# Performance work log

Measured on AMD Instinct MI355X. Metric: run time of the kernel, lower is better.

## Reference

```python
import jax, jax.numpy as jnp
import numpy as np

B, S, D = 2, 2048, 1024
H, DK = 16, 64  # n_heads, d_k == d_v


def setup_inputs() -> dict:
    key = jax.random.key(0)
    ks = jax.random.split(key, 12)
    sd = 1.0 / np.sqrt(D)
    inp = {
        "Q": jax.random.normal(ks[0], (B, S, D), jnp.float32),
        "K": jax.random.normal(ks[1], (B, S, D), jnp.float32),
        "V": jax.random.normal(ks[2], (B, S, D), jnp.float32),
        "attn_mask": jax.random.randint(ks[3], (B, S, S), 0, 2).astype(bool),
        "Wq": jax.random.normal(ks[4], (D, H * DK), jnp.float32) * sd,
        "bq": jnp.zeros((H * DK,), jnp.float32),
        "Wk": jax.random.normal(ks[5], (D, H * DK), jnp.float32) * sd,
        "bk": jnp.zeros((H * DK,), jnp.float32),
        "Wv": jax.random.normal(ks[6], (D, H * DK), jnp.float32) * sd,
        "bv": jnp.zeros((H * DK,), jnp.float32),
        "Wo": jax.random.normal(ks[7], (H * DK, D), jnp.float32) * sd,
        "bo": jnp.zeros((D,), jnp.float32),
        "ln_g": jnp.ones((D,), jnp.float32),
        "ln_b": jnp.zeros((D,), jnp.float32),
    }
    return inp


def _layer_norm(x, g, b, eps=1e-5):
    mu = jnp.mean(x, axis=-1, keepdims=True)
    var = jnp.var(x, axis=-1, keepdims=True)
    return (x - mu) * jax.lax.rsqrt(var + eps) * g + b


def reference(Q, K, V, attn_mask, Wq, bq, Wk, bk, Wv, bv, Wo, bo, ln_g, ln_b):
    # NOTE: faithful to the source — K and V projections are computed from Q.
    residual = Q
    q = (Q @ Wq + bq).reshape(B, S, H, DK).transpose(0, 2, 1, 3)  # [B,H,S,DK]
    k = (Q @ Wk + bk).reshape(B, S, H, DK).transpose(0, 2, 1, 3)
    v = (Q @ Wv + bv).reshape(B, S, H, DK).transpose(0, 2, 1, 3)
    scale = 1.0 / np.sqrt(DK)
    scores = jnp.einsum("bhqd,bhkd->bhqk", q, k) * scale  # [B,H,S,S]
    scores = jnp.where(attn_mask[:, None, :, :], jnp.float32(-1e9), scores)
    attn = jax.nn.softmax(scores, axis=-1)
    context = jnp.einsum("bhqk,bhkd->bhqd", attn, v)
    context = context.transpose(0, 2, 1, 3).reshape(B, S, H * DK)
    output = context @ Wo + bo
    return _layer_norm(output + residual, ln_g, ln_b), attn
```

## Files before the change

kernel.cpp:

```cpp
#include <hip/hip_runtime.h>
#include <stdint.h>

typedef unsigned short u16;
typedef short bf16x8 __attribute__((ext_vector_type(8)));
typedef float f32x4 __attribute__((ext_vector_type(4)));

static __device__ __forceinline__ u16 f2b(float f) {
    uint32_t u = __float_as_uint(f);
    uint32_t r = (u + 0x7fffu + ((u >> 16) & 1u)) >> 16;
    return (u16)r;
}
static __device__ __forceinline__ float b2f(u16 u) {
    union { float f; uint32_t i; } x; x.i = ((uint32_t)u) << 16; return x.f;
}

#define GLOAD16(g, l)                                                        \
    __builtin_amdgcn_global_load_lds(                                        \
        (const __attribute__((address_space(1))) uint32_t*)(g),              \
        (__attribute__((address_space(3))) uint32_t*)(l), 16, 0, 0)

__global__ __launch_bounds__(256) void pack_mask_k(const int* __restrict__ mask,
                                                   unsigned long long* __restrict__ bits) {
    const int row = blockIdx.x;
    const int wave = threadIdx.x >> 6, lane = threadIdx.x & 63;
    const int* mrow = mask + (size_t)row * 2048;
#pragma unroll
    for (int it = 0; it < 8; ++it) {
        int col = it * 256 + threadIdx.x;
        unsigned long long b = __ballot(mrow[col] != 0);
        if (lane == 0) bits[(size_t)row * 32 + it * 4 + wave] = b;
    }
}

__global__ __launch_bounds__(256) void transpose_w_k(const float* __restrict__ Wq, const float* __restrict__ Wk,
                                                     const float* __restrict__ Wv, const float* __restrict__ Wo,
                                                     u16* __restrict__ WtAll) {
    __shared__ u16 t[32][36];
    const float* W = blockIdx.z == 0 ? Wq : blockIdx.z == 1 ? Wk : blockIdx.z == 2 ? Wv : Wo;
    u16* out = WtAll + (size_t)blockIdx.z * (1024u * 1024u);
    const int r = threadIdx.x >> 3, c4 = (threadIdx.x & 7) * 4;
    float4 v = *(const float4*)(W + (size_t)(blockIdx.y * 32 + r) * 1024 + blockIdx.x * 32 + c4);
    t[r][c4 + 0] = f2b(v.x); t[r][c4 + 1] = f2b(v.y); t[r][c4 + 2] = f2b(v.z); t[r][c4 + 3] = f2b(v.w);
    __syncthreads();
    ushort4 o;
    o.x = t[c4 + 0][r]; o.y = t[c4 + 1][r]; o.z = t[c4 + 2][r]; o.w = t[c4 + 3][r];
    *(ushort4*)(out + (size_t)(blockIdx.x * 32 + r) * 1024 + blockIdx.y * 32 + c4) = o;
}

__global__ __launch_bounds__(256) void qcvt_k(const float* __restrict__ Q, u16* __restrict__ qbf) {
    const size_t i = ((size_t)blockIdx.x * 256 + threadIdx.x) * 8;
    float4 a = *(const float4*)(Q + i);
    float4 b = *(const float4*)(Q + i + 4);
    bf16x8 o;
    o[0] = (short)f2b(a.x); o[1] = (short)f2b(a.y); o[2] = (short)f2b(a.z); o[3] = (short)f2b(a.w);
    o[4] = (short)f2b(b.x); o[5] = (short)f2b(b.y); o[6] = (short)f2b(b.z); o[7] = (short)f2b(b.w);
    *(bf16x8*)(qbf + i) = o;
}

__global__ __launch_bounds__(256) void gemm_qkv_k(const u16* __restrict__ Abf, const u16* __restrict__ WtAll,
                                                  const float* __restrict__ bq, const float* __restrict__ bk,
                                                  const float* __restrict__ bv,
                                                  u16* __restrict__ q_ws, u16* __restrict__ k_ws,
                                                  u16* __restrict__ v_ws) {
    __shared__ u16 Asm[128 * 32];
    __shared__ u16 Bsm[128 * 32];
    const int tid = threadIdx.x;
    const int wave = tid >> 6, lane = tid & 63, quad = lane >> 4, l16 = lane & 15;
    const int wr = wave >> 1, wc = wave & 1;
    const int m0 = blockIdx.y * 128, n0 = blockIdx.x * 128;

    const u16* Ag = Abf + (size_t)(m0 + (tid >> 2)) * 1024 + (tid & 3) * 8;
    const u16* Bg = WtAll + (size_t)(n0 + (tid >> 2)) * 1024 + (tid & 3) * 8;

    const f32x4 zero = {0.f, 0.f, 0.f, 0.f};
    f32x4 acc[4][4];
#pragma unroll
    for (int i = 0; i < 4; ++i)
#pragma unroll
        for (int j = 0; j < 4; ++j) acc[i][j] = zero;

    for (int k0 = 0; k0 < 1024; k0 += 32) {
        GLOAD16(Ag + k0, &Asm[tid * 8]);
        GLOAD16(Ag + k0 + (size_t)64 * 1024, &Asm[2048 + tid * 8]);
        GLOAD16(Bg + k0, &Bsm[tid * 8]);
        GLOAD16(Bg + k0 + (size_t)64 * 1024, &Bsm[2048 + tid * 8]);
        __syncthreads();
        bf16x8 a[4], b[4];
#pragma unroll
        for (int i = 0; i < 4; ++i) {
            a[i] = *(const bf16x8*)&Asm[(wr * 64 + i * 16 + l16) * 32 + quad * 8];
            b[i] = *(const bf16x8*)&Bsm[(wc * 64 + i * 16 + l16) * 32 + quad * 8];
        }
#pragma unroll
        for (int mi = 0; mi < 4; ++mi)
#pragma unroll
            for (int ni = 0; ni < 4; ++ni)
                acc[mi][ni] = __builtin_amdgcn_mfma_f32_16x16x32_bf16(a[mi], b[ni], acc[mi][ni], 0, 0, 0);
        __syncthreads();
    }

    const int z = n0 >> 10;
    const float* bias = z == 0 ? bq : z == 1 ? bk : bv;
    u16* out = z == 0 ? q_ws : z == 1 ? k_ws : v_ws;
    const float oscale = (z == 0) ? 0.18033688011112042f : 1.0f;
#pragma unroll
    for (int ni = 0; ni < 4; ++ni) {
        const int n = n0 + wc * 64 + ni * 16 + l16;
        const int nn = n & 1023, h = nn >> 6, d = nn & 63;
        const float bsf = bias[nn];
#pragma unroll
        for (int mi = 0; mi < 4; ++mi)
#pragma unroll
            for (int r = 0; r < 4; ++r) {
                const int m = m0 + wr * 64 + mi * 16 + quad * 4 + r;
                const int bb = m >> 11, s = m & 2047;
                out[((size_t)(bb * 16 + h) * 2048 + s) * 64 + d] = f2b((acc[mi][ni][r] + bsf) * oscale);
            }
    }
}

__global__ __launch_bounds__(256) void vtr_k(const u16* __restrict__ v_ws, u16* __restrict__ vT) {
    __shared__ u16 t[32][36];
    const int bh = blockIdx.z, s0 = blockIdx.x * 32, d0 = blockIdx.y * 32;
    const int r = threadIdx.x >> 3, c4 = (threadIdx.x & 7) * 4;
    ushort4 v = *(const ushort4*)(v_ws + ((size_t)bh * 2048 + s0 + r) * 64 + d0 + c4);
    t[r][c4 + 0] = v.x; t[r][c4 + 1] = v.y; t[r][c4 + 2] = v.z; t[r][c4 + 3] = v.w;
    __syncthreads();
    ushort4 o;
    o.x = t[c4 + 0][r]; o.y = t[c4 + 1][r]; o.z = t[c4 + 2][r]; o.w = t[c4 + 3][r];
    *(ushort4*)(vT + ((size_t)bh * 64 + d0 + r) * 2048 + s0 + c4) = o;
}

__global__ __launch_bounds__(256) void attn_k(const u16* __restrict__ q_ws, const u16* __restrict__ k_ws,
                                              const u16* __restrict__ vT,
                                              const unsigned long long* __restrict__ mbits,
                                              float* __restrict__ attn_out, u16* __restrict__ ctx_ws) {
    const int bh = blockIdx.y, b = bh >> 4, h = bh & 15;
    const int q0 = blockIdx.x * 64;
    const int tid = threadIdx.x;
    const int wave = tid >> 6, lane = tid & 63, quad = lane >> 4, l16 = lane & 15;

    __shared__ u16 Ksm[64][72];
    __shared__ u16 Vsm[64][72];
    __shared__ u16 Psm[4][16][72];

    const u16* qp = q_ws + ((size_t)bh * 2048 + q0 + wave * 16 + l16) * 64;
    const bf16x8 aq0 = *(const bf16x8*)(qp + quad * 8);
    const bf16x8 aq1 = *(const bf16x8*)(qp + 32 + quad * 8);

    const size_t mbase = ((size_t)b * 2048 + q0 + wave * 16 + quad * 4) * 32;

    const int r0 = tid >> 3, c0 = (tid & 7) * 8;
    const u16* kgb = k_ws + (size_t)bh * 2048 * 64;
    const u16* vtg = vT + (size_t)bh * 64 * 2048;

    const f32x4 zero = {0.f, 0.f, 0.f, 0.f};
    float lsum[4] = {0.f, 0.f, 0.f, 0.f};

    for (int kt = 0; kt < 32; ++kt) {
        const int s0 = kt * 64;
        *(bf16x8*)&Ksm[r0][c0] = *(const bf16x8*)(kgb + (size_t)(s0 + r0) * 64 + c0);
        *(bf16x8*)&Ksm[r0 + 32][c0] = *(const bf16x8*)(kgb + (size_t)(s0 + r0 + 32) * 64 + c0);
        __syncthreads();
        f32x4 sc[4];
#pragma unroll
        for (int nt = 0; nt < 4; ++nt) {
            sc[nt] = zero;
            bf16x8 bk0 = *(const bf16x8*)&Ksm[nt * 16 + l16][quad * 8];
            bf16x8 bk1 = *(const bf16x8*)&Ksm[nt * 16 + l16][32 + quad * 8];
            sc[nt] = __builtin_amdgcn_mfma_f32_16x16x32_bf16(aq0, bk0, sc[nt], 0, 0, 0);
            sc[nt] = __builtin_amdgcn_mfma_f32_16x16x32_bf16(aq1, bk1, sc[nt], 0, 0, 0);
        }
        unsigned long long mw[4];
#pragma unroll
        for (int r = 0; r < 4; ++r) mw[r] = mbits[mbase + (size_t)r * 32 + kt];
#pragma unroll
        for (int nt = 0; nt < 4; ++nt)
#pragma unroll
            for (int r = 0; r < 4; ++r) {
                const int bit = (int)((mw[r] >> (nt * 16 + l16)) & 1ull);
                lsum[r] += bit ? 0.f : exp2f(sc[nt][r]);
            }
        __syncthreads();
    }
#pragma unroll
    for (int r = 0; r < 4; ++r) {
#pragma unroll
        for (int off = 1; off < 16; off <<= 1) lsum[r] += __shfl_xor(lsum[r], off, 64);
    }
    float rl[4];
#pragma unroll
    for (int r = 0; r < 4; ++r) rl[r] = 1.0f / lsum[r];

    f32x4 cacc[4];
#pragma unroll
    for (int i = 0; i < 4; ++i) cacc[i] = zero;

    for (int kt = 0; kt < 32; ++kt) {
        const int s0 = kt * 64;
        *(bf16x8*)&Ksm[r0][c0] = *(const bf16x8*)(kgb + (size_t)(s0 + r0) * 64 + c0);
        *(bf16x8*)&Ksm[r0 + 32][c0] = *(const bf16x8*)(kgb + (size_t)(s0 + r0 + 32) * 64 + c0);
        *(bf16x8*)&Vsm[r0][c0] = *(const bf16x8*)(vtg + (size_t)r0 * 2048 + s0 + c0);
        *(bf16x8*)&Vsm[r0 + 32][c0] = *(const bf16x8*)(vtg + (size_t)(r0 + 32) * 2048 + s0 + c0);
        __syncthreads();

        f32x4 sc[4];
#pragma unroll
        for (int nt = 0; nt < 4; ++nt) {
            sc[nt] = zero;
            bf16x8 bk0 = *(const bf16x8*)&Ksm[nt * 16 + l16][quad * 8];
            bf16x8 bk1 = *(const bf16x8*)&Ksm[nt * 16 + l16][32 + quad * 8];
            sc[nt] = __builtin_amdgcn_mfma_f32_16x16x32_bf16(aq0, bk0, sc[nt], 0, 0, 0);
            sc[nt] = __builtin_amdgcn_mfma_f32_16x16x32_bf16(aq1, bk1, sc[nt], 0, 0, 0);
        }
        unsigned long long mw[4];
#pragma unroll
        for (int r = 0; r < 4; ++r) mw[r] = mbits[mbase + (size_t)r * 32 + kt];
#pragma unroll
        for (int nt = 0; nt < 4; ++nt)
#pragma unroll
            for (int r = 0; r < 4; ++r) {
                const int bit = (int)((mw[r] >> (nt * 16 + l16)) & 1ull);
                const float p = bit ? 0.f : exp2f(sc[nt][r]) * rl[r];
                Psm[wave][quad * 4 + r][nt * 16 + l16] = f2b(p);
            }
#pragma unroll
        for (int j = 0; j < 4; ++j) {
            const int pr = j * 4 + (lane >> 4), pc = (lane & 15) * 4;
            ushort4 pv = *(const ushort4*)&Psm[wave][pr][pc];
            float4 pf;
            pf.x = b2f(pv.x); pf.y = b2f(pv.y); pf.z = b2f(pv.z); pf.w = b2f(pv.w);
            float* ap = attn_out + ((size_t)bh * 2048 + q0 + wave * 16 + pr) * 2048 + s0 + pc;
            *(float4*)ap = pf;
        }
        bf16x8 pa0 = *(const bf16x8*)&Psm[wave][l16][quad * 8];
        bf16x8 pa1 = *(const bf16x8*)&Psm[wave][l16][32 + quad * 8];
#pragma unroll
        for (int dt = 0; dt < 4; ++dt) {
            bf16x8 bv0 = *(const bf16x8*)&Vsm[dt * 16 + l16][quad * 8];
            bf16x8 bv1 = *(const bf16x8*)&Vsm[dt * 16 + l16][32 + quad * 8];
            cacc[dt] = __builtin_amdgcn_mfma_f32_16x16x32_bf16(pa0, bv0, cacc[dt], 0, 0, 0);
            cacc[dt] = __builtin_amdgcn_mfma_f32_16x16x32_bf16(pa1, bv1, cacc[dt], 0, 0, 0);
        }
        __syncthreads();
    }

#pragma unroll
    for (int dt = 0; dt < 4; ++dt) {
        const int d = dt * 16 + l16;
#pragma unroll
        for (int r = 0; r < 4; ++r) {
            const int s = q0 + wave * 16 + quad * 4 + r;
            ctx_ws[((size_t)b * 2048 + s) * 1024 + h * 64 + d] = f2b(cacc[dt][r]);
        }
    }
}

__global__ __launch_bounds__(256) void out_proj_k(const u16* __restrict__ Ctx, const u16* __restrict__ WtO,
                                                  const float* __restrict__ bo, const float* __restrict__ Qin,
                                                  float* __restrict__ ln_in) {
    __shared__ u16 Asm[128 * 32];
    __shared__ u16 Bsm[128 * 32];
    const int tid = threadIdx.x;
    const int wave = tid >> 6, lane = tid & 63, quad = lane >> 4, l16 = lane & 15;
    const int wr = wave >> 1, wc = wave & 1;
    const int m0 = blockIdx.y * 128, n0 = blockIdx.x * 128;

    const u16* Ag = Ctx + (size_t)(m0 + (tid >> 2)) * 1024 + (tid & 3) * 8;
    const u16* Bg = WtO + (size_t)(n0 + (tid >> 2)) * 1024 + (tid & 3) * 8;

    const f32x4 zero = {0.f, 0.f, 0.f, 0.f};
    f32x4 acc[4][4];
#pragma unroll
    for (int i = 0; i < 4; ++i)
#pragma unroll
        for (int j = 0; j < 4; ++j) acc[i][j] = zero;

    for (int k0 = 0; k0 < 1024; k0 += 32) {
        GLOAD16(Ag + k0, &Asm[tid * 8]);
        GLOAD16(Ag + k0 + (size_t)64 * 1024, &Asm[2048 + tid * 8]);
        GLOAD16(Bg + k0, &Bsm[tid * 8]);
        GLOAD16(Bg + k0 + (size_t)64 * 1024, &Bsm[2048 + tid * 8]);
        __syncthreads();
        bf16x8 a[4], b[4];
#pragma unroll
        for (int i = 0; i < 4; ++i) {
            a[i] = *(const bf16x8*)&Asm[(wr * 64 + i * 16 + l16) * 32 + quad * 8];
            b[i] = *(const bf16x8*)&Bsm[(wc * 64 + i * 16 + l16) * 32 + quad * 8];
        }
#pragma unroll
        for (int mi = 0; mi < 4; ++mi)
#pragma unroll
            for (int ni = 0; ni < 4; ++ni)
                acc[mi][ni] = __builtin_amdgcn_mfma_f32_16x16x32_bf16(a[mi], b[ni], acc[mi][ni], 0, 0, 0);
        __syncthreads();
    }
#pragma unroll
    for (int ni = 0; ni < 4; ++ni) {
        const int n = n0 + wc * 64 + ni * 16 + l16;
        const float bsf = bo[n];
#pragma unroll
        for (int mi = 0; mi < 4; ++mi)
#pragma unroll
            for (int r = 0; r < 4; ++r) {
                const int m = m0 + wr * 64 + mi * 16 + quad * 4 + r;
                ln_in[(size_t)m * 1024 + n] = acc[mi][ni][r] + bsf + Qin[(size_t)m * 1024 + n];
            }
    }
}

__global__ __launch_bounds__(256) void layernorm_k(const float* __restrict__ x, const float* __restrict__ g,
                                                   const float* __restrict__ bta, float* __restrict__ out) {
    const int row = blockIdx.x, tid = threadIdx.x;
    const float4 v = *(const float4*)(x + (size_t)row * 1024 + tid * 4);
    float s = v.x + v.y + v.z + v.w;
    float sq = v.x * v.x + v.y * v.y + v.z * v.z + v.w * v.w;
#pragma unroll
    for (int off = 32; off; off >>= 1) {
        s += __shfl_xor(s, off, 64);
        sq += __shfl_xor(sq, off, 64);
    }
    __shared__ float ss[4], ssq[4];
    const int wave = tid >> 6, lane = tid & 63;
    if (lane == 0) { ss[wave] = s; ssq[wave] = sq; }
    __syncthreads();
    const float S = ss[0] + ss[1] + ss[2] + ss[3];
    const float SQ = ssq[0] + ssq[1] + ssq[2] + ssq[3];
    const float mu = S * (1.f / 1024.f);
    const float rs = rsqrtf(SQ * (1.f / 1024.f) - mu * mu + 1e-5f);
    const float* vf = (const float*)&v;
    float4 o;
    float tmp[4];
#pragma unroll
    for (int j = 0; j < 4; ++j) {
        const int c = tid * 4 + j;
        tmp[j] = (vf[j] - mu) * rs * g[c] + bta[c];
    }
    o.x = tmp[0]; o.y = tmp[1]; o.z = tmp[2]; o.w = tmp[3];
    *(float4*)(out + (size_t)row * 1024 + tid * 4) = o;
}

extern "C" void kernel_launch(void* const* d_in, const int* in_sizes, int n_in,
                              void* d_out, int out_size, void* d_ws, size_t ws_size,
                              hipStream_t stream) {
    const float* Q  = (const float*)d_in[0];
    const int* mask = (const int*)d_in[3];
    const float* Wq = (const float*)d_in[4];
    const float* bq = (const float*)d_in[5];
    const float* Wk = (const float*)d_in[6];
    const float* bk = (const float*)d_in[7];
    const float* Wv = (const float*)d_in[8];
    const float* bv = (const float*)d_in[9];
    const float* Wo = (const float*)d_in[10];
    const float* bo = (const float*)d_in[11];
    const float* g  = (const float*)d_in[12];
    const float* be = (const float*)d_in[13];

    char* ws = (char*)d_ws;
    u16* WtAll = (u16*)(ws);
    u16* q_ws  = (u16*)(ws + ((size_t)8  << 20));
    u16* k_ws  = (u16*)(ws + ((size_t)16 << 20));
    u16* v_ws  = (u16*)(ws + ((size_t)24 << 20));
    u16* c_ws  = (u16*)(ws + ((size_t)32 << 20));
    u16* qbf   = (u16*)(ws + ((size_t)40 << 20));
    u16* vT    = (u16*)(ws + ((size_t)40 << 20));
    float* ln_in = (float*)(ws + ((size_t)40 << 20));
    unsigned long long* mbits = (unsigned long long*)(ws + ((size_t)56 << 20));

    float* out_ln = (float*)d_out;
    float* out_at = (float*)d_out + (size_t)2 * 2048 * 1024;

    transpose_w_k<<<dim3(32, 32, 4), dim3(256), 0, stream>>>(Wq, Wk, Wv, Wo, WtAll);
    pack_mask_k<<<dim3(4096), dim3(256), 0, stream>>>(mask, mbits);
    qcvt_k<<<dim3(2048), dim3(256), 0, stream>>>(Q, qbf);
    gemm_qkv_k<<<dim3(24, 32), dim3(256), 0, stream>>>(qbf, WtAll, bq, bk, bv, q_ws, k_ws, v_ws);
    vtr_k<<<dim3(64, 2, 32), dim3(256), 0, stream>>>(v_ws, vT);
    attn_k<<<dim3(32, 32), dim3(256), 0, stream>>>(q_ws, k_ws, vT, mbits, out_at, c_ws);
    out_proj_k<<<dim3(8, 32), dim3(256), 0, stream>>>(c_ws, WtAll + (size_t)3 * 1024 * 1024, bo, Q, ln_in);
    layernorm_k<<<dim3(4096), dim3(256), 0, stream>>>(ln_in, g, be, out_ln);
    (void)in_sizes; (void)n_in; (void)out_size; (void)ws_size;
}
```

Measured before the change: 837.5 us.

## Load K/V MFMA operands directly from global, drop LDS staging and barriers

The attention kernel no longer stages K and transposed V tiles through shared memory with __syncthreads. Each wave now loads its MFMA B-operands straight from global memory, counting on L1/L2 to serve the data that all four waves share. The grid mapping is swapped so that consecutive blocks cover the same batch-head, which should improve L2 reuse of K and V. s_setprio is raised around the MFMA sections. The risk is extra global/L1 traffic and exposed load latency with no explicit prefetch, in exchange for removing barrier stalls and LDS traffic.

```diff
diff --git a/kernel.cpp b/kernel.cpp
--- a/kernel.cpp
+++ b/kernel.cpp
@@ -135,13 +135,11 @@
                                               const u16* __restrict__ vT,
                                               const unsigned long long* __restrict__ mbits,
                                               float* __restrict__ attn_out, u16* __restrict__ ctx_ws) {
-    const int bh = blockIdx.y, b = bh >> 4, h = bh & 15;
-    const int q0 = blockIdx.x * 64;
+    const int bh = blockIdx.x, b = bh >> 4;
+    const int q0 = blockIdx.y * 64;
     const int tid = threadIdx.x;
     const int wave = tid >> 6, lane = tid & 63, quad = lane >> 4, l16 = lane & 15;
 
-    __shared__ u16 Ksm[64][72];
-    __shared__ u16 Vsm[64][72];
     __shared__ u16 Psm[4][16][72];
 
     const u16* qp = q_ws + ((size_t)bh * 2048 + q0 + wave * 16 + l16) * 64;
@@ -150,7 +148,6 @@
 
     const size_t mbase = ((size_t)b * 2048 + q0 + wave * 16 + quad * 4) * 32;
 
-    const int r0 = tid >> 3, c0 = (tid & 7) * 8;
     const u16* kgb = k_ws + (size_t)bh * 2048 * 64;
     const u16* vtg = vT + (size_t)bh * 64 * 2048;
 
@@ -158,19 +155,18 @@
     float lsum[4] = {0.f, 0.f, 0.f, 0.f};
 
     for (int kt = 0; kt < 32; ++kt) {
-        const int s0 = kt * 64;
-        *(bf16x8*)&Ksm[r0][c0] = *(const bf16x8*)(kgb + (size_t)(s0 + r0) * 64 + c0);
-        *(bf16x8*)&Ksm[r0 + 32][c0] = *(const bf16x8*)(kgb + (size_t)(s0 + r0 + 32) * 64 + c0);
-        __syncthreads();
+        const u16* kp = kgb + (size_t)kt * 64 * 64 + (size_t)l16 * 64 + quad * 8;
         f32x4 sc[4];
+        __builtin_amdgcn_s_setprio(1);
 #pragma unroll
         for (int nt = 0; nt < 4; ++nt) {
+            bf16x8 bk0 = *(const bf16x8*)(kp + nt * 1024);
+            bf16x8 bk1 = *(const bf16x8*)(kp + nt * 1024 + 32);
             sc[nt] = zero;
-            bf16x8 bk0 = *(const bf16x8*)&Ksm[nt * 16 + l16][quad * 8];
-            bf16x8 bk1 = *(const bf16x8*)&Ksm[nt * 16 + l16][32 + quad * 8];
             sc[nt] = __builtin_amdgcn_mfma_f32_16x16x32_bf16(aq0, bk0, sc[nt], 0, 0, 0);
             sc[nt] = __builtin_amdgcn_mfma_f32_16x16x32_bf16(aq1, bk1, sc[nt], 0, 0, 0);
         }
+        __builtin_amdgcn_s_setprio(0);
         unsigned long long mw[4];
 #pragma unroll
         for (int r = 0; r < 4; ++r) mw[r] = mbits[mbase + (size_t)r * 32 + kt];
@@ -181,7 +177,6 @@
                 const int bit = (int)((mw[r] >> (nt * 16 + l16)) & 1ull);
                 lsum[r] += bit ? 0.f : exp2f(sc[nt][r]);
             }
-        __syncthreads();
     }
 #pragma unroll
     for (int r = 0; r < 4; ++r) {
@@ -198,21 +193,18 @@
 
     for (int kt = 0; kt < 32; ++kt) {
         const int s0 = kt * 64;
-        *(bf16x8*)&Ksm[r0][c0] = *(const bf16x8*)(kgb + (size_t)(s0 + r0) * 64 + c0);
-        *(bf16x8*)&Ksm[r0 + 32][c0] = *(const bf16x8*)(kgb + (size_t)(s0 + r0 + 32) * 64 + c0);
-        *(bf16x8*)&Vsm[r0][c0] = *(const bf16x8*)(vtg + (size_t)r0 * 2048 + s0 + c0);
-        *(bf16x8*)&Vsm[r0 + 32][c0] = *(const bf16x8*)(vtg + (size_t)(r0 + 32) * 2048 + s0 + c0);
-        __syncthreads();
-
+        const u16* kp = kgb + (size_t)s0 * 64 + (size_t)l16 * 64 + quad * 8;
         f32x4 sc[4];
+        __builtin_amdgcn_s_setprio(1);
 #pragma unroll
         for (int nt = 0; nt < 4; ++nt) {
+            bf16x8 bk0 = *(const bf16x8*)(kp + nt * 1024);
+            bf16x8 bk1 = *(const bf16x8*)(kp + nt * 1024 + 32);
             sc[nt] = zero;
-            bf16x8 bk0 = *(const bf16x8*)&Ksm[nt * 16 + l16][quad * 8];
-            bf16x8 bk1 = *(const bf16x8*)&Ksm[nt * 16 + l16][32 + quad * 8];
             sc[nt] = __builtin_amdgcn_mfma_f32_16x16x32_bf16(aq0, bk0, sc[nt], 0, 0, 0);
             sc[nt] = __builtin_amdgcn_mfma_f32_16x16x32_bf16(aq1, bk1, sc[nt], 0, 0, 0);
         }
+        __builtin_amdgcn_s_setprio(0);
         unsigned long long mw[4];
 #pragma unroll
         for (int r = 0; r < 4; ++r) mw[r] = mbits[mbase + (size_t)r * 32 + kt];
@@ -235,16 +227,19 @@
         }
         bf16x8 pa0 = *(const bf16x8*)&Psm[wave][l16][quad * 8];
         bf16x8 pa1 = *(const bf16x8*)&Psm[wave][l16][32 + quad * 8];
+        const u16* vp = vtg + (size_t)l16 * 2048 + s0 + quad * 8;
+        __builtin_amdgcn_s_setprio(1);
 #pragma unroll
         for (int dt = 0; dt < 4; ++dt) {
-            bf16x8 bv0 = *(const bf16x8*)&Vsm[dt * 16 + l16][quad * 8];
-            bf16x8 bv1 = *(const bf16x8*)&Vsm[dt * 16 + l16][32 + quad * 8];
+            bf16x8 bv0 = *(const bf16x8*)(vp + (size_t)dt * 16 * 2048);
+            bf16x8 bv1 = *(const bf16x8*)(vp + (size_t)dt * 16 * 2048 + 32);
             cacc[dt] = __builtin_amdgcn_mfma_f32_16x16x32_bf16(pa0, bv0, cacc[dt], 0, 0, 0);
             cacc[dt] = __builtin_amdgcn_mfma_f32_16x16x32_bf16(pa1, bv1, cacc[dt], 0, 0, 0);
         }
-        __syncthreads();
-    }
-
+        __builtin_amdgcn_s_setprio(0);
+    }
+
+    const int h = bh & 15;
 #pragma unroll
     for (int dt = 0; dt < 4; ++dt) {
         const int d = dt * 16 + l16;
```

Result: slower. 1.109 ms (+32.4%).

## Double-buffer K/V tiles via async global-to-LDS loads with XOR swizzle

Applied to the files above, without the earlier changes.

Replaces the register-staged K and V tile loads in the attention kernel with global_load_lds copies into double-buffered, XOR-swizzled LDS tiles. The next tile is prefetched while the current one is consumed, which is meant to hide global load latency. The unpadded layout relies on the swizzle to avoid LDS bank conflicts. The grid axes are also swapped so consecutive blocks walk heads first, which changes L2 locality for the mask bits and K/V. There is one barrier per iteration, and the async copy relies on that barrier for ordering. This may race if the loads are not waited on (vmcnt) before the barrier.

```diff
diff --git a/kernel.cpp b/kernel.cpp
--- a/kernel.cpp
+++ b/kernel.cpp
@@ -131,18 +131,42 @@
     *(ushort4*)(vT + ((size_t)bh * 64 + d0 + r) * 2048 + s0 + c4) = o;
 }
 
+static __device__ __forceinline__ bf16x8 ld_swz(const u16* tile, int row, int cb) {
+    const int off = row * 128 + (cb ^ ((row & 7) << 4));
+    return *(const bf16x8*)((const char*)tile + off);
+}
+
 __global__ __launch_bounds__(256) void attn_k(const u16* __restrict__ q_ws, const u16* __restrict__ k_ws,
                                               const u16* __restrict__ vT,
                                               const unsigned long long* __restrict__ mbits,
                                               float* __restrict__ attn_out, u16* __restrict__ ctx_ws) {
-    const int bh = blockIdx.y, b = bh >> 4, h = bh & 15;
-    const int q0 = blockIdx.x * 64;
+    const int bh = blockIdx.x, b = bh >> 4, h = bh & 15;
+    const int q0 = blockIdx.y * 64;
     const int tid = threadIdx.x;
     const int wave = tid >> 6, lane = tid & 63, quad = lane >> 4, l16 = lane & 15;
 
-    __shared__ u16 Ksm[64][72];
-    __shared__ u16 Vsm[64][72];
+    __shared__ u16 Ksm[2][64 * 64];
+    __shared__ u16 Vsm[2][64 * 64];
     __shared__ u16 Psm[4][16][72];
+
+    const int st_row = tid >> 3;
+    const int st_sw = ((tid & 7) * 16) ^ ((st_row & 7) << 4);
+
+    const char* kgb = (const char*)(k_ws + (size_t)bh * 2048 * 64);
+    const char* vgb = (const char*)(vT + (size_t)bh * 64 * 2048);
+
+#define STAGE_K(buf, kt)                                                                   \
+    {                                                                                      \
+        const char* _s = kgb + (size_t)(kt) * 8192 + (size_t)st_row * 128 + st_sw;         \
+        GLOAD16(_s, &Ksm[buf][tid * 8]);                                                   \
+        GLOAD16(_s + 32 * 128, &Ksm[buf][2048 + tid * 8]);                                 \
+    }
+#define STAGE_V(buf, kt)                                                                   \
+    {                                                                                      \
+        const char* _s = vgb + (size_t)(kt) * 128 + (size_t)st_row * 4096 + st_sw;         \
+        GLOAD16(_s, &Vsm[buf][tid * 8]);                                                   \
+        GLOAD16(_s + (size_t)32 * 4096, &Vsm[buf][2048 + tid * 8]);                        \
+    }
 
     const u16* qp = q_ws + ((size_t)bh * 2048 + q0 + wave * 16 + l16) * 64;
     const bf16x8 aq0 = *(const bf16x8*)(qp + quad * 8);
@@ -150,24 +174,20 @@
 
     const size_t mbase = ((size_t)b * 2048 + q0 + wave * 16 + quad * 4) * 32;
 
-    const int r0 = tid >> 3, c0 = (tid & 7) * 8;
-    const u16* kgb = k_ws + (size_t)bh * 2048 * 64;
-    const u16* vtg = vT + (size_t)bh * 64 * 2048;
-
     const f32x4 zero = {0.f, 0.f, 0.f, 0.f};
     float lsum[4] = {0.f, 0.f, 0.f, 0.f};
 
+    STAGE_K(0, 0);
+    __syncthreads();
     for (int kt = 0; kt < 32; ++kt) {
-        const int s0 = kt * 64;
-        *(bf16x8*)&Ksm[r0][c0] = *(const bf16x8*)(kgb + (size_t)(s0 + r0) * 64 + c0);
-        *(bf16x8*)&Ksm[r0 + 32][c0] = *(const bf16x8*)(kgb + (size_t)(s0 + r0 + 32) * 64 + c0);
-        __syncthreads();
+        const int cur = kt & 1;
+        if (kt < 31) STAGE_K(cur ^ 1, kt + 1);
         f32x4 sc[4];
 #pragma unroll
         for (int nt = 0; nt < 4; ++nt) {
+            bf16x8 bk0 = ld_swz(Ksm[cur], nt * 16 + l16, quad * 16);
+            bf16x8 bk1 = ld_swz(Ksm[cur], nt * 16 + l16, 64 + quad * 16);
             sc[nt] = zero;
-            bf16x8 bk0 = *(const bf16x8*)&Ksm[nt * 16 + l16][quad * 8];
-            bf16x8 bk1 = *(const bf16x8*)&Ksm[nt * 16 + l16][32 + quad * 8];
             sc[nt] = __builtin_amdgcn_mfma_f32_16x16x32_bf16(aq0, bk0, sc[nt], 0, 0, 0);
             sc[nt] = __builtin_amdgcn_mfma_f32_16x16x32_bf16(aq1, bk1, sc[nt], 0, 0, 0);
         }
@@ -196,20 +216,22 @@
 #pragma unroll
     for (int i = 0; i < 4; ++i) cacc[i] = zero;
 
+    STAGE_K(0, 0);
+    STAGE_V(0, 0);
+    __syncthreads();
     for (int kt = 0; kt < 32; ++kt) {
+        const int cur = kt & 1;
         const int s0 = kt * 64;
-        *(bf16x8*)&Ksm[r0][c0] = *(const bf16x8*)(kgb + (size_t)(s0 + r0) * 64 + c0);
-        *(bf16x8*)&Ksm[r0 + 32][c0] = *(const bf16x8*)(kgb + (size_t)(s0 + r0 + 32) * 64 + c0);
-        *(bf16x8*)&Vsm[r0][c0] = *(const bf16x8*)(vtg + (size_t)r0 * 2048 + s0 + c0);
-        *(bf16x8*)&Vsm[r0 + 32][c0] = *(const bf16x8*)(vtg + (size_t)(r0 + 32) * 2048 + s0 + c0);
-        __syncthreads();
-
+        if (kt < 31) {
+            STAGE_K(cur ^ 1, kt + 1);
+            STAGE_V(cur ^ 1, kt + 1);
+        }
         f32x4 sc[4];
 #pragma unroll
         for (int nt = 0; nt < 4; ++nt) {
+            bf16x8 bk0 = ld_swz(Ksm[cur], nt * 16 + l16, quad * 16);
+            bf16x8 bk1 = ld_swz(Ksm[cur], nt * 16 + l16, 64 + quad * 16);
             sc[nt] = zero;
-            bf16x8 bk0 = *(const bf16x8*)&Ksm[nt * 16 + l16][quad * 8];
-            bf16x8 bk1 = *(const bf16x8*)&Ksm[nt * 16 + l16][32 + quad * 8];
             sc[nt] = __builtin_amdgcn_mfma_f32_16x16x32_bf16(aq0, bk0, sc[nt], 0, 0, 0);
             sc[nt] = __builtin_amdgcn_mfma_f32_16x16x32_bf16(aq1, bk1, sc[nt], 0, 0, 0);
         }
@@ -237,13 +259,15 @@
         bf16x8 pa1 = *(const bf16x8*)&Psm[wave][l16][32 + quad * 8];
 #pragma unroll
         for (int dt = 0; dt < 4; ++dt) {
-            bf16x8 bv0 = *(const bf16x8*)&Vsm[dt * 16 + l16][quad * 8];
-            bf16x8 bv1 = *(const bf16x8*)&Vsm[dt * 16 + l16][32 + quad * 8];
+            bf16x8 bv0 = ld_swz(Vsm[cur], dt * 16 + l16, quad * 16);
+            bf16x8 bv1 = ld_swz(Vsm[cur], dt * 16 + l16, 64 + quad * 16);
             cacc[dt] = __builtin_amdgcn_mfma_f32_16x16x32_bf16(pa0, bv0, cacc[dt], 0, 0, 0);
             cacc[dt] = __builtin_amdgcn_mfma_f32_16x16x32_bf16(pa1, bv1, cacc[dt], 0, 0, 0);
         }
         __syncthreads();
     }
+#undef STAGE_K
+#undef STAGE_V
 
 #pragma unroll
     for (int dt = 0; dt < 4; ++dt) {
```

After: 842.8 us. About the same (+0.6%).
